# Kernel tuning notes

Hardware: AMD Instinct MI355X
Metric: run time of the kernel (lower is better)

The kernel has to match this reference:

```python
import jax, jax.numpy as jnp
import numpy as np

N = 1500
GAT_IN = 32
GAT_OUT = 8
MLP_HIDDEN = 128
ALPHA = 0.2  # leaky relu slope
NEG_INF = -9.0e15


def setup_inputs() -> dict:
    key = jax.random.key(0)
    ks = jax.random.split(key, 16)
    eye = jnp.eye(N, dtype=jnp.float32)
    geo_adj = jnp.maximum((jax.random.uniform(ks[0], (N, N)) < 0.02).astype(jnp.float32), eye)
    sem_adj = jnp.maximum((jax.random.uniform(ks[1], (N, N)) < 0.02).astype(jnp.float32), eye)
    features = jax.random.normal(ks[2], (N, GAT_IN), dtype=jnp.float32)
    # all (i, j) region pairs, as in the original source
    ii, jj = jnp.meshgrid(jnp.arange(N), jnp.arange(N), indexing='ij')
    region_pairs = jnp.stack([ii.reshape(-1), jj.reshape(-1)], axis=1).astype(jnp.int64)
    distance_features = jax.random.uniform(ks[3], (N * N, 1), dtype=jnp.float32)
    def lin(k, fan_in, fan_out):
        return jax.random.normal(k, (fan_in, fan_out), dtype=jnp.float32) / jnp.sqrt(jnp.float32(fan_in))
    W0 = lin(ks[4], GAT_IN, GAT_OUT)
    W1 = lin(ks[5], GAT_OUT, GAT_OUT)
    W2 = lin(ks[6], GAT_OUT, GAT_OUT)
    a0 = lin(ks[7], 2 * GAT_OUT, 1)
    a1 = lin(ks[8], 2 * GAT_OUT, 1)
    a2 = lin(ks[9], 2 * GAT_OUT, 1)
    fc1_w = lin(ks[10], 2 * GAT_OUT + 1, MLP_HIDDEN)
    fc1_b = jnp.zeros((MLP_HIDDEN,), dtype=jnp.float32)
    fc2_w = lin(ks[11], MLP_HIDDEN, 1)
    fc2_b = jnp.zeros((1,), dtype=jnp.float32)
    return {"geo_adj": geo_adj, "sem_adj": sem_adj, "features": features,
            "region_pairs": region_pairs, "distance_features": distance_features,
            "W0": W0, "W1": W1, "W2": W2, "a0": a0, "a1": a1, "a2": a2,
            "fc1_w": fc1_w, "fc1_b": fc1_b, "fc2_w": fc2_w, "fc2_b": fc2_b}


def _gat_layer(combined_adj, feats, W, a):
    # h = W feats; attention score a([h_i || h_j]) decomposes into h_i@a1 + h_j@a2
    h = feats @ W                      # [N, out]
    f_src = h @ a[:GAT_OUT]            # [N, 1]
    f_dst = h @ a[GAT_OUT:]            # [N, 1]
    e = jax.nn.leaky_relu(f_src + f_dst.T, negative_slope=ALPHA)  # [N, N]
    e = e * combined_adj
    att = jax.nn.softmax(jnp.where(combined_adj > 0, e, NEG_INF), axis=1)
    return jax.nn.elu(att @ h)


def reference(geo_adj, sem_adj, features, region_pairs, distance_features,
              W0, W1, W2, a0, a1, a2, fc1_w, fc1_b, fc2_w, fc2_b):
    combined_adj = geo_adj + sem_adj
    enc = features
    for W, a in ((W0, a0), (W1, a1), (W2, a2)):
        enc = _gat_layer(combined_adj, enc, W, a)
    r1 = enc[region_pairs[:, 0]]       # [N^2, out]
    r2 = enc[region_pairs[:, 1]]       # [N^2, out]
    comb = jnp.concatenate([r1, r2, distance_features], axis=1)  # [N^2, 17]
    hid = jax.nn.relu(comb @ fc1_w + fc1_b)
    return hid @ fc2_w + fc2_b
```

## Files before the change

kernel.cpp:

```cpp
#include <hip/hip_runtime.h>
#include <hip/hip_bf16.h>

#define NN 1500
#define GIN 32
#define GOUT 8
#define HID 128
#define CAP 192

__global__ void gat_first(const float* __restrict__ geo,
                          const float* __restrict__ sem,
                          const float* __restrict__ feat,
                          const float* __restrict__ W0,
                          const float* __restrict__ a0,
                          int* __restrict__ csr_idx,
                          float* __restrict__ csr_val,
                          int* __restrict__ csr_cnt,
                          float* __restrict__ enc_out) {
    const int i = blockIdx.x;
    const int t = threadIdx.x;
    __shared__ int cnt;
    __shared__ int sidx[CAP];
    __shared__ float sval[CAP];
    __shared__ float hi_s[GOUT];
    __shared__ float wsum[4][GOUT + 1];
    if (t == 0) cnt = 0;
    __syncthreads();

    const float* grow = geo + (size_t)i * NN;
    const float* srow = sem + (size_t)i * NN;
    for (int q = t; q < NN / 4; q += 256) {
        float4 g = *(const float4*)(grow + 4 * q);
        float4 s = *(const float4*)(srow + 4 * q);
        float a[4] = {g.x + s.x, g.y + s.y, g.z + s.z, g.w + s.w};
        #pragma unroll
        for (int c = 0; c < 4; ++c) {
            if (a[c] > 0.f) {
                int p = atomicAdd(&cnt, 1);
                if (p < CAP) { sidx[p] = 4 * q + c; sval[p] = a[c]; }
            }
        }
    }
    if (t < GOUT) {
        float hv = 0.f;
        #pragma unroll 4
        for (int c = 0; c < GIN; ++c)
            hv = fmaf(feat[(size_t)i * GIN + c], W0[c * GOUT + t], hv);
        hi_s[t] = hv;
    }
    __syncthreads();

    const int c2 = cnt < CAP ? cnt : CAP;
    if (t == 0) csr_cnt[i] = c2;
    for (int p = t; p < c2; p += 256) {
        csr_idx[(size_t)i * CAP + p] = sidx[p];
        csr_val[(size_t)i * CAP + p] = sval[p];
    }
    float fsrc = 0.f;
    #pragma unroll
    for (int k = 0; k < GOUT; ++k) fsrc = fmaf(hi_s[k], a0[k], fsrc);

    float den = 0.f;
    float num[GOUT] = {};
    if (t < c2) {
        int j = sidx[t];
        float a = sval[t];
        float hj[GOUT] = {};
        #pragma unroll
        for (int c4 = 0; c4 < GIN / 4; ++c4) {
            float4 e4 = *(const float4*)(feat + (size_t)j * GIN + 4 * c4);
            const float* ep = (const float*)&e4;
            #pragma unroll
            for (int c = 0; c < 4; ++c)
                #pragma unroll
                for (int k = 0; k < GOUT; ++k)
                    hj[k] = fmaf(ep[c], W0[(4 * c4 + c) * GOUT + k], hj[k]);
        }
        float fd = 0.f;
        #pragma unroll
        for (int k = 0; k < GOUT; ++k) fd = fmaf(hj[k], a0[GOUT + k], fd);
        float ev = fsrc + fd;
        ev = (ev > 0.f) ? ev : 0.2f * ev;
        ev *= a;
        float p = __expf(ev);
        den = p;
        #pragma unroll
        for (int k = 0; k < GOUT; ++k) num[k] = p * hj[k];
    }
    #pragma unroll
    for (int off = 32; off > 0; off >>= 1) {
        den += __shfl_xor(den, off, 64);
        #pragma unroll
        for (int k = 0; k < GOUT; ++k) num[k] += __shfl_xor(num[k], off, 64);
    }
    if ((t & 63) == 0) {
        wsum[t >> 6][0] = den;
        #pragma unroll
        for (int k = 0; k < GOUT; ++k) wsum[t >> 6][1 + k] = num[k];
    }
    __syncthreads();
    if (t < GOUT) {
        float L = wsum[0][0] + wsum[1][0] + wsum[2][0] + wsum[3][0];
        float v = (wsum[0][1 + t] + wsum[1][1 + t] + wsum[2][1 + t] + wsum[3][1 + t]) / L;
        enc_out[(size_t)i * GOUT + t] = (v > 0.f) ? v : (__expf(v) - 1.f);
    }
}

template<int IN, bool UV>
__global__ void gat_layer(const float* __restrict__ enc,
                          const float* __restrict__ W,
                          const float* __restrict__ avec,
                          const int* __restrict__ csr_idx,
                          const float* __restrict__ csr_val,
                          const int* __restrict__ csr_cnt,
                          float* __restrict__ enc_out,
                          const float* __restrict__ fc1w,
                          const float* __restrict__ fc1b,
                          const float* __restrict__ fc2w,
                          float* __restrict__ Ubuf, float* __restrict__ Vbuf,
                          float* __restrict__ Arow, float* __restrict__ Bcol,
                          float* __restrict__ cptr) {
    const int tid = threadIdx.x;
    const int lane = tid & 63;
    const int i = blockIdx.x * 4 + (tid >> 6);

    float hv = 0.f;
    if (lane < GOUT) {
        #pragma unroll 4
        for (int c = 0; c < IN; ++c)
            hv = fmaf(enc[(size_t)i * IN + c], W[c * GOUT + lane], hv);
    }
    float hi[GOUT];
    #pragma unroll
    for (int c = 0; c < GOUT; ++c) hi[c] = __shfl(hv, c, 64);
    float fsrc = 0.f;
    #pragma unroll
    for (int c = 0; c < GOUT; ++c) fsrc = fmaf(hi[c], avec[c], fsrc);

    const int cnt = csr_cnt[i];
    float den = 0.f;
    float num[GOUT] = {};
    for (int e = lane; e < cnt; e += 64) {
        int j = csr_idx[(size_t)i * CAP + e];
        float a = csr_val[(size_t)i * CAP + e];
        float hj[GOUT] = {};
        #pragma unroll
        for (int c4 = 0; c4 < IN / 4; ++c4) {
            float4 e4 = *(const float4*)(enc + (size_t)j * IN + 4 * c4);
            const float* ep = (const float*)&e4;
            #pragma unroll
            for (int c = 0; c < 4; ++c)
                #pragma unroll
                for (int k = 0; k < GOUT; ++k)
                    hj[k] = fmaf(ep[c], W[(4 * c4 + c) * GOUT + k], hj[k]);
        }
        float fd = 0.f;
        #pragma unroll
        for (int k = 0; k < GOUT; ++k) fd = fmaf(hj[k], avec[GOUT + k], fd);
        float ev = fsrc + fd;
        ev = (ev > 0.f) ? ev : 0.2f * ev;
        ev *= a;
        float p = __expf(ev);
        den += p;
        #pragma unroll
        for (int k = 0; k < GOUT; ++k) num[k] = fmaf(p, hj[k], num[k]);
    }
    #pragma unroll
    for (int off = 32; off > 0; off >>= 1) {
        den += __shfl_xor(den, off, 64);
        #pragma unroll
        for (int k = 0; k < GOUT; ++k) num[k] += __shfl_xor(num[k], off, 64);
    }
    float vout = 0.f;
    if (lane < GOUT) {
        float v = num[lane] / den;
        vout = (v > 0.f) ? v : (__expf(v) - 1.f);
        enc_out[(size_t)i * GOUT + lane] = vout;
    }

    if constexpr (UV) {
        float er[GOUT];
        #pragma unroll
        for (int c = 0; c < GOUT; ++c) er[c] = __shfl(vout, c, 64);
        const int kl = lane, kh = lane + 64;
        float u_lo = fc1b[kl], u_hi = fc1b[kh];
        float v_lo = 0.f, v_hi = 0.f;
        #pragma unroll
        for (int c = 0; c < GOUT; ++c) {
            u_lo = fmaf(er[c], fc1w[c * HID + kl], u_lo);
            u_hi = fmaf(er[c], fc1w[c * HID + kh], u_hi);
            v_lo = fmaf(er[c], fc1w[(GOUT + c) * HID + kl], v_lo);
            v_hi = fmaf(er[c], fc1w[(GOUT + c) * HID + kh], v_hi);
        }
        Ubuf[(size_t)i * HID + kl] = u_lo;
        Ubuf[(size_t)i * HID + kh] = u_hi;
        Vbuf[(size_t)i * HID + kl] = v_lo;
        Vbuf[(size_t)i * HID + kh] = v_hi;
        const float f_lo = fc2w[kl], f_hi = fc2w[kh];
        float ap = u_lo * f_lo + u_hi * f_hi;
        float bp = v_lo * f_lo + v_hi * f_hi;
        #pragma unroll
        for (int off = 32; off > 0; off >>= 1) {
            ap += __shfl_xor(ap, off, 64);
            bp += __shfl_xor(bp, off, 64);
        }
        if (lane == 0) { Arow[i] = ap; Bcol[i] = bp; }
        if (i == 0) {
            const float* w16g = fc1w + 2 * GOUT * HID;
            float cp = w16g[kl] * f_lo + w16g[kh] * f_hi;
            #pragma unroll
            for (int off = 32; off > 0; off >>= 1) cp += __shfl_xor(cp, off, 64);
            if (lane == 0) cptr[0] = cp;
        }
    }
}

#define BT 64
#define KS 64
#define KSTR 68

__global__ __launch_bounds__(256, 4) void mlp_kernel(
        const float* __restrict__ U, const float* __restrict__ V,
        const float* __restrict__ Arow, const float* __restrict__ Bcol,
        const float* __restrict__ cptr,
        const float* __restrict__ dist,
        const float* __restrict__ fc1w,
        const float* __restrict__ fc2w,
        const float* __restrict__ fc2b,
        float* __restrict__ out) {
    __shared__ float Us[BT * KSTR];
    __shared__ float Vs[BT * KSTR];

    const int tid = threadIdx.x;
    const int i0 = blockIdx.y * BT;
    const int j0 = blockIdx.x * BT;
    const int tx = tid & 15;
    const int ty = tid >> 4;

    const float* w16g = fc1w + 2 * GOUT * HID;

    int irow[4], jcol[4];
    float d[4][4];
    #pragma unroll
    for (int ii = 0; ii < 4; ++ii) irow[ii] = i0 + ty + 16 * ii;
    #pragma unroll
    for (int jj = 0; jj < 4; ++jj) jcol[jj] = j0 + tx + 16 * jj;
    #pragma unroll
    for (int ii = 0; ii < 4; ++ii) {
        int ic = irow[ii] < NN ? irow[ii] : NN - 1;
        #pragma unroll
        for (int jj = 0; jj < 4; ++jj) {
            int jc = jcol[jj] < NN ? jcol[jj] : NN - 1;
            d[ii][jj] = dist[(size_t)ic * NN + jc];
        }
    }

    float acc[4][4] = {};

    #pragma unroll
    for (int ph = 0; ph < 2; ++ph) {
        const int k0 = ph * KS;
        if (ph) __syncthreads();
        for (int u = tid; u < 2 * BT * 16; u += 256) {
            const int isU = (u < BT * 16);
            const int q = isU ? u : u - BT * 16;
            const int r = q >> 4;
            const int kq = (q & 15) << 2;
            int g = (isU ? i0 : j0) + r;
            if (g >= NN) g = NN - 1;
            float4 val = *(const float4*)((isU ? U : V) + (size_t)g * HID + k0 + kq);
            *(float4*)((isU ? Us : Vs) + r * KSTR + kq) = val;
        }
        __syncthreads();

        #pragma unroll 2
        for (int k4 = 0; k4 < KS; k4 += 4) {
            float4 u4[4], v4[4];
            #pragma unroll
            for (int ii = 0; ii < 4; ++ii)
                u4[ii] = *(const float4*)(Us + (ty + 16 * ii) * KSTR + k4);
            #pragma unroll
            for (int jj = 0; jj < 4; ++jj)
                v4[jj] = *(const float4*)(Vs + (tx + 16 * jj) * KSTR + k4);
            float wv[4], fv[4];
            #pragma unroll
            for (int kk = 0; kk < 4; ++kk) {
                wv[kk] = w16g[k0 + k4 + kk];
                fv[kk] = fc2w[k0 + k4 + kk];
            }
            #pragma unroll
            for (int kk = 0; kk < 4; ++kk) {
                #pragma unroll
                for (int ii = 0; ii < 4; ++ii) {
                    float uk = ((const float*)&u4[ii])[kk];
                    #pragma unroll
                    for (int jj = 0; jj < 4; ++jj) {
                        float t = fmaf(d[ii][jj], wv[kk],
                                       uk + ((const float*)&v4[jj])[kk]);
                        acc[ii][jj] = fmaf(fabsf(t), fv[kk], acc[ii][jj]);
                    }
                }
            }
        }
    }

    const float c = cptr[0];
    const float b2 = fc2b[0];
    #pragma unroll
    for (int ii = 0; ii < 4; ++ii) {
        if (irow[ii] >= NN) continue;
        const float Ai = Arow[irow[ii]];
        #pragma unroll
        for (int jj = 0; jj < 4; ++jj) {
            if (jcol[jj] >= NN) continue;
            float lin = Ai + Bcol[jcol[jj]] + d[ii][jj] * c;
            out[(size_t)irow[ii] * NN + jcol[jj]] = fmaf(0.5f, lin + acc[ii][jj], b2);
        }
    }
}

extern "C" void kernel_launch(void* const* d_in, const int* in_sizes, int n_in,
                              void* d_out, int out_size, void* d_ws, size_t ws_size,
                              hipStream_t stream) {
    const float* geo  = (const float*)d_in[0];
    const float* sem  = (const float*)d_in[1];
    const float* feat = (const float*)d_in[2];
    const float* dist = (const float*)d_in[4];
    const float* W0   = (const float*)d_in[5];
    const float* W1   = (const float*)d_in[6];
    const float* W2   = (const float*)d_in[7];
    const float* a0   = (const float*)d_in[8];
    const float* a1   = (const float*)d_in[9];
    const float* a2   = (const float*)d_in[10];
    const float* fc1w = (const float*)d_in[11];
    const float* fc1b = (const float*)d_in[12];
    const float* fc2w = (const float*)d_in[13];
    const float* fc2b = (const float*)d_in[14];
    float* out = (float*)d_out;

    char* ws = (char*)d_ws;
    int*   csr_idx = (int*)ws;                         ws += sizeof(int) * NN * CAP;
    float* csr_val = (float*)ws;                       ws += sizeof(float) * NN * CAP;
    int*   csr_cnt = (int*)ws;                         ws += sizeof(int) * NN;
    float* encA    = (float*)ws;                       ws += sizeof(float) * NN * GOUT;
    float* encB    = (float*)ws;                       ws += sizeof(float) * NN * GOUT;
    float* Ubuf    = (float*)ws;                       ws += sizeof(float) * NN * HID;
    float* Vbuf    = (float*)ws;                       ws += sizeof(float) * NN * HID;
    float* Ar      = (float*)ws;                       ws += sizeof(float) * NN;
    float* Bc      = (float*)ws;                       ws += sizeof(float) * NN;
    float* cptr    = (float*)ws;

    gat_first<<<NN, 256, 0, stream>>>(geo, sem, feat, W0, a0,
                                      csr_idx, csr_val, csr_cnt, encA);
    gat_layer<GOUT, false><<<NN / 4, 256, 0, stream>>>(
        encA, W1, a1, csr_idx, csr_val, csr_cnt, encB,
        nullptr, nullptr, nullptr, nullptr, nullptr, nullptr, nullptr, nullptr);
    gat_layer<GOUT, true><<<NN / 4, 256, 0, stream>>>(
        encB, W2, a2, csr_idx, csr_val, csr_cnt, encA,
        fc1w, fc1b, fc2w, Ubuf, Vbuf, Ar, Bc, cptr);

    dim3 mg((NN + BT - 1) / BT, (NN + BT - 1) / BT);
    mlp_kernel<<<mg, 256, 0, stream>>>(Ubuf, Vbuf, Ar, Bc, cptr,
                                       dist, fc1w, fc2w, fc2b, out);
}
```

Measured before the change: 169.6 us.

## Restructure MLP kernel to per-thread column with broadcast U rows, no LDS

Replaces the 64x64 LDS-tiled MLP kernel with one where each thread owns a single output column j and 12 rows i. The thread reads its V row directly from global memory, and the U rows are wave-uniform loads that get broadcast. This removes the shared-memory staging and barriers, and gives coalesced stores along j. In exchange, V is re-read from global or cache by every thread, U is re-fetched per chunk, and output blocks past column 1500 are wasted (6 blocks of 256 cover 1536 columns). Since 1500 = 12 × 125, IB=12 divides NN exactly and no row bounds check is needed.

Result: faster. 156.9 us (-7.5%).

```diff
diff --git a/kernel.cpp b/kernel.cpp
--- a/kernel.cpp
+++ b/kernel.cpp
@@ -214,9 +214,8 @@
     }
 }
 
-#define BT 64
-#define KS 64
-#define KSTR 68
+#define IB 12
+#define KC 16
 
 __global__ __launch_bounds__(256, 4) void mlp_kernel(
         const float* __restrict__ U, const float* __restrict__ V,
@@ -227,93 +226,56 @@
         const float* __restrict__ fc2w,
         const float* __restrict__ fc2b,
         float* __restrict__ out) {
-    __shared__ float Us[BT * KSTR];
-    __shared__ float Vs[BT * KSTR];
-
     const int tid = threadIdx.x;
-    const int i0 = blockIdx.y * BT;
-    const int j0 = blockIdx.x * BT;
-    const int tx = tid & 15;
-    const int ty = tid >> 4;
-
+    const int j = blockIdx.x * 256 + tid;
+    const int jc = j < NN ? j : NN - 1;
+    const int i0 = blockIdx.y * IB;
     const float* w16g = fc1w + 2 * GOUT * HID;
 
-    int irow[4], jcol[4];
-    float d[4][4];
-    #pragma unroll
-    for (int ii = 0; ii < 4; ++ii) irow[ii] = i0 + ty + 16 * ii;
-    #pragma unroll
-    for (int jj = 0; jj < 4; ++jj) jcol[jj] = j0 + tx + 16 * jj;
-    #pragma unroll
-    for (int ii = 0; ii < 4; ++ii) {
-        int ic = irow[ii] < NN ? irow[ii] : NN - 1;
-        #pragma unroll
-        for (int jj = 0; jj < 4; ++jj) {
-            int jc = jcol[jj] < NN ? jcol[jj] : NN - 1;
-            d[ii][jj] = dist[(size_t)ic * NN + jc];
-        }
-    }
-
-    float acc[4][4] = {};
-
-    #pragma unroll
-    for (int ph = 0; ph < 2; ++ph) {
-        const int k0 = ph * KS;
-        if (ph) __syncthreads();
-        for (int u = tid; u < 2 * BT * 16; u += 256) {
-            const int isU = (u < BT * 16);
-            const int q = isU ? u : u - BT * 16;
-            const int r = q >> 4;
-            const int kq = (q & 15) << 2;
-            int g = (isU ? i0 : j0) + r;
-            if (g >= NN) g = NN - 1;
-            float4 val = *(const float4*)((isU ? U : V) + (size_t)g * HID + k0 + kq);
-            *(float4*)((isU ? Us : Vs) + r * KSTR + kq) = val;
-        }
-        __syncthreads();
-
-        #pragma unroll 2
-        for (int k4 = 0; k4 < KS; k4 += 4) {
-            float4 u4[4], v4[4];
+    float d[IB], acc[IB];
+    #pragma unroll
+    for (int r = 0; r < IB; ++r) {
+        d[r] = dist[(size_t)(i0 + r) * NN + jc];
+        acc[r] = 0.f;
+    }
+
+    const float* Vrow = V + (size_t)jc * HID;
+    for (int kc = 0; kc < HID; kc += KC) {
+        float v[KC];
+        #pragma unroll
+        for (int q = 0; q < KC; q += 4)
+            *(float4*)(v + q) = *(const float4*)(Vrow + kc + q);
+        float wv[KC], fv[KC];
+        #pragma unroll
+        for (int q = 0; q < KC; q += 4) {
+            *(float4*)(wv + q) = *(const float4*)(w16g + kc + q);
+            *(float4*)(fv + q) = *(const float4*)(fc2w + kc + q);
+        }
+        #pragma unroll
+        for (int r = 0; r < IB; ++r) {
+            const float* Urow = U + (size_t)(i0 + r) * HID + kc;
             #pragma unroll
-            for (int ii = 0; ii < 4; ++ii)
-                u4[ii] = *(const float4*)(Us + (ty + 16 * ii) * KSTR + k4);
-            #pragma unroll
-            for (int jj = 0; jj < 4; ++jj)
-                v4[jj] = *(const float4*)(Vs + (tx + 16 * jj) * KSTR + k4);
-            float wv[4], fv[4];
-            #pragma unroll
-            for (int kk = 0; kk < 4; ++kk) {
-                wv[kk] = w16g[k0 + k4 + kk];
-                fv[kk] = fc2w[k0 + k4 + kk];
-            }
-            #pragma unroll
-            for (int kk = 0; kk < 4; ++kk) {
+            for (int q = 0; q < KC; q += 4) {
+                float4 u4 = *(const float4*)(Urow + q);
+                const float* up = (const float*)&u4;
                 #pragma unroll
-                for (int ii = 0; ii < 4; ++ii) {
-                    float uk = ((const float*)&u4[ii])[kk];
-                    #pragma unroll
-                    for (int jj = 0; jj < 4; ++jj) {
-                        float t = fmaf(d[ii][jj], wv[kk],
-                                       uk + ((const float*)&v4[jj])[kk]);
-                        acc[ii][jj] = fmaf(fabsf(t), fv[kk], acc[ii][jj]);
-                    }
+                for (int k = 0; k < 4; ++k) {
+                    float t = up[k] + v[q + k];
+                    t = fmaf(d[r], wv[q + k], t);
+                    acc[r] = fmaf(__builtin_fabsf(t), fv[q + k], acc[r]);
                 }
             }
         }
     }
 
-    const float c = cptr[0];
-    const float b2 = fc2b[0];
-    #pragma unroll
-    for (int ii = 0; ii < 4; ++ii) {
-        if (irow[ii] >= NN) continue;
-        const float Ai = Arow[irow[ii]];
-        #pragma unroll
-        for (int jj = 0; jj < 4; ++jj) {
-            if (jcol[jj] >= NN) continue;
-            float lin = Ai + Bcol[jcol[jj]] + d[ii][jj] * c;
-            out[(size_t)irow[ii] * NN + jcol[jj]] = fmaf(0.5f, lin + acc[ii][jj], b2);
+    if (j < NN) {
+        const float c = cptr[0];
+        const float b2 = fc2b[0];
+        const float Bj = Bcol[jc];
+        #pragma unroll
+        for (int r = 0; r < IB; ++r) {
+            float lin = Arow[i0 + r] + Bj + d[r] * c;
+            out[(size_t)(i0 + r) * NN + j] = fmaf(0.5f, lin + acc[r], b2);
         }
     }
 }
@@ -358,7 +320,7 @@
         encB, W2, a2, csr_idx, csr_val, csr_cnt, encA,
         fc1w, fc1b, fc2w, Ubuf, Vbuf, Ar, Bc, cptr);
 
-    dim3 mg((NN + BT - 1) / BT, (NN + BT - 1) / BT);
+    dim3 mg((NN + 255) / 256, (NN + IB - 1) / IB);
     mlp_kernel<<<mg, 256, 0, stream>>>(Ubuf, Vbuf, Ar, Bc, cptr,
                                        dist, fc1w, fc2w, fc2b, out);
 }
```
